# Kernel optimization log

Measured on AMD Instinct MI355X. Metric: run time of the kernel, lower is better.

## Reference

```python
import jax, jax.numpy as jnp
import numpy as np

N_NODES = 100000
N_EDGES = 1600000
N_GRAPHS = 512


def gcn_conv(x, W, b, src, dst, n_nodes):
    """GCNConv with self-loops: D^-1/2 (A+I) D^-1/2 X W + b."""
    h = x @ W  # [N, out]
    ones = jnp.ones((src.shape[0],), h.dtype)
    deg = jax.ops.segment_sum(ones, dst, num_segments=n_nodes) + 1.0  # +1 self-loop
    dinv = jax.lax.rsqrt(deg)
    norm = dinv[src] * dinv[dst]  # [E]
    agg = jax.ops.segment_sum(h[src] * norm[:, None], dst, num_segments=n_nodes)
    agg = agg + h * (1.0 / deg)[:, None]  # self-loop term: deg^-0.5 * deg^-0.5
    return agg + b


def setup_inputs() -> dict:
    key = jax.random.key(0)
    ks = jax.random.split(key, 12)
    x = jax.random.normal(ks[0], (N_NODES, 78), dtype=jnp.float32)
    edge_index = jax.random.randint(ks[1], (2, N_EDGES), 0, N_NODES, dtype=jnp.int64)
    batch = jnp.sort(jax.random.randint(ks[2], (N_NODES,), 0, N_GRAPHS, dtype=jnp.int64))
    def glorot(k, shape):
        lim = np.sqrt(6.0 / (shape[0] + shape[1])).astype(np.float32)
        return jax.random.uniform(k, shape, jnp.float32, -lim, lim)
    return {
        "x": x,
        "edge_index": edge_index,
        "batch": batch,
        "W1": glorot(ks[3], (78, 128)),
        "b1": jnp.zeros((128,), jnp.float32),
        "W2": glorot(ks[4], (128, 256)),
        "b2": jnp.zeros((256,), jnp.float32),
        "Wg1": glorot(ks[5], (256, 1024)),
        "bg1": jnp.zeros((1024,), jnp.float32),
        "Wg2": glorot(ks[6], (1024, 128)),
        "bg2": jnp.zeros((128,), jnp.float32),
    }


def reference(x, edge_index, batch, W1, b1, W2, b2, Wg1, bg1, Wg2, bg2):
    src, dst = edge_index[0], edge_index[1]
    n = x.shape[0]
    h = jax.nn.relu(gcn_conv(x, W1, b1, src, dst, n))   # [N,128]
    h = jax.nn.relu(gcn_conv(h, W2, b2, src, dst, n))   # [N,256]
    g = jax.ops.segment_max(h, batch, num_segments=N_GRAPHS)  # global max pool [G,256]
    g = jax.nn.relu(g @ Wg1 + bg1)   # [G,1024]; dropout is identity at eval
    g = g @ Wg2 + bg2                # [G,128]
    return g
```

## Files before the change

kernel.cpp:

```cpp
#include <hip/hip_runtime.h>
#include <hip/hip_fp16.h>


#define NN 100000
#define NE 1600000
#define NG 512
#define NBLK ((NN + 1023) / 1024)

typedef float v2f __attribute__((ext_vector_type(2)));


__global__ void k_hist(const int* __restrict__ dst, int* cnt, int e) {
    int i = blockIdx.x * blockDim.x + threadIdx.x;
    if (i < e) atomicAdd(&cnt[dst[i]], 1);
}

__global__ void k_prep(const int* __restrict__ cnt, float* __restrict__ dinv,
                       float* __restrict__ gmax) {
    int i = blockIdx.x * blockDim.x + threadIdx.x;
    if (i < NN) dinv[i] = rsqrtf((float)cnt[i] + 1.0f);
    if (i < NG * 256) gmax[i] = 0.0f;
}

__global__ void k_cvt_x(const float* __restrict__ x, __half* __restrict__ xh) {
    int i = blockIdx.x * blockDim.x + threadIdx.x;
    if (i < NN * 39) {
        float2 v = ((const float2*)x)[i];
        ((__half2*)xh)[i] = __floats2half2_rn(v.x, v.y);
    }
}

__global__ __launch_bounds__(256) void k_bsum(const int* __restrict__ cnt, int* __restrict__ bsum) {
    __shared__ int s[256];
    int b = blockIdx.x, t = threadIdx.x;
    int base = b * 1024 + t * 4;
    int v = 0;
#pragma unroll
    for (int j = 0; j < 4; j++) { int i = base + j; if (i < NN) v += cnt[i]; }
    s[t] = v; __syncthreads();
    for (int off = 128; off > 0; off >>= 1) {
        if (t < off) s[t] += s[t + off];
        __syncthreads();
    }
    if (t == 0) bsum[b] = s[0];
}

__global__ __launch_bounds__(128) void k_scan_bsum(int* bsum, int* row_ptr) {
    __shared__ int s[128];
    int t = threadIdx.x;
    int v = (t < NBLK) ? bsum[t] : 0;
    s[t] = v; __syncthreads();
    for (int off = 1; off < 128; off <<= 1) {
        int u = (t >= off) ? s[t - off] : 0;
        __syncthreads();
        s[t] += u;
        __syncthreads();
    }
    if (t < NBLK) bsum[t] = s[t] - v;
    if (t == 0) row_ptr[NN] = NE;
}

__global__ __launch_bounds__(256) void k_scan_blocks(const int* __restrict__ cnt,
    const int* __restrict__ bsum, int* __restrict__ row_ptr, int* __restrict__ cursor) {
    __shared__ int s[256];
    int b = blockIdx.x, t = threadIdx.x;
    int base = b * 1024 + t * 4;
    int v[4]; int sum = 0;
#pragma unroll
    for (int j = 0; j < 4; j++) { int i = base + j; v[j] = (i < NN) ? cnt[i] : 0; sum += v[j]; }
    s[t] = sum; __syncthreads();
    for (int off = 1; off < 256; off <<= 1) {
        int u = (t >= off) ? s[t - off] : 0;
        __syncthreads();
        s[t] += u;
        __syncthreads();
    }
    int excl = s[t] - sum + bsum[b];
#pragma unroll
    for (int j = 0; j < 4; j++) {
        int i = base + j;
        if (i < NN) { row_ptr[i] = excl; cursor[i] = excl; excl += v[j]; }
    }
}

__global__ void k_fillslots(const int* __restrict__ src, const int* __restrict__ dst,
    const float* __restrict__ dinv, int* cursor, int2* __restrict__ es, int e) {
    int i = blockIdx.x * blockDim.x + threadIdx.x;
    if (i >= e) return;
    int s = src[i], d = dst[i];
    int pos = atomicAdd(&cursor[d], 1);
    es[pos] = make_int2(s, __float_as_int(dinv[s] * dinv[d]));
}

__global__ __launch_bounds__(256) void k_fused1(const __half* __restrict__ x,
    const int* __restrict__ rp, const int2* __restrict__ es,
    const float* __restrict__ dinv, const float* __restrict__ W,
    const float* __restrict__ bias, __half* __restrict__ out) {
    __shared__ float As[4][8][80];
    int tid = threadIdx.x;
    int wv = tid >> 6, l = tid & 63;
    int task = __builtin_amdgcn_readfirstlane(blockIdx.x * 4 + wv);
    int n0 = task * 8;
    if (n0 >= NN) return;

    if (l < 39) {
        for (int pi = 0; pi < 4; pi++) {
            int nA = n0 + 2 * pi, nB = nA + 1;
            float diA = dinv[nA], swA = diA * diA;
            float diB = dinv[nB], swB = diB * diB;
            float2 aA = __half22float2(((const __half2*)(x + (size_t)nA * 78))[l]);
            float2 aB = __half22float2(((const __half2*)(x + (size_t)nB * 78))[l]);
            aA.x *= swA; aA.y *= swA;
            aB.x *= swB; aB.y *= swB;
            int eA = rp[nA], eA1 = rp[nA + 1];
            int eB = rp[nB], eB1 = rp[nB + 1];
            int cA = (eA1 - eA) >> 3, cB = (eB1 - eB) >> 3;
            while (cA > 0 || cB > 0) {
                bool dA = (cA > 0), dB = (cB > 0);
                int2 esA[8], esB[8];
                __half2 vA[8], vB[8];
                if (dA) {
#pragma unroll
                    for (int j = 0; j < 8; j++) esA[j] = es[eA + j];
                }
                if (dB) {
#pragma unroll
                    for (int j = 0; j < 8; j++) esB[j] = es[eB + j];
                }
                if (dA) {
#pragma unroll
                    for (int j = 0; j < 8; j++)
                        vA[j] = ((const __half2*)(x + (size_t)esA[j].x * 78))[l];
                }
                if (dB) {
#pragma unroll
                    for (int j = 0; j < 8; j++)
                        vB[j] = ((const __half2*)(x + (size_t)esB[j].x * 78))[l];
                }
                if (dA) {
#pragma unroll
                    for (int j = 0; j < 8; j++) {
                        float w = __int_as_float(esA[j].y);
                        float2 v = __half22float2(vA[j]);
                        aA.x += v.x * w; aA.y += v.y * w;
                    }
                    eA += 8; cA--;
                }
                if (dB) {
#pragma unroll
                    for (int j = 0; j < 8; j++) {
                        float w = __int_as_float(esB[j].y);
                        float2 v = __half22float2(vB[j]);
                        aB.x += v.x * w; aB.y += v.y * w;
                    }
                    eB += 8; cB--;
                }
            }
            while (eA < eA1 && eB < eB1) {
                int2 pA = es[eA], pB = es[eB];
                float2 vA2 = __half22float2(((const __half2*)(x + (size_t)pA.x * 78))[l]);
                float2 vB2 = __half22float2(((const __half2*)(x + (size_t)pB.x * 78))[l]);
                float wA = __int_as_float(pA.y), wB = __int_as_float(pB.y);
                aA.x += vA2.x * wA; aA.y += vA2.y * wA;
                aB.x += vB2.x * wB; aB.y += vB2.y * wB;
                eA++; eB++;
            }
            for (; eA < eA1; eA++) {
                int2 p = es[eA];
                float w = __int_as_float(p.y);
                float2 v = __half22float2(((const __half2*)(x + (size_t)p.x * 78))[l]);
                aA.x += v.x * w; aA.y += v.y * w;
            }
            for (; eB < eB1; eB++) {
                int2 p = es[eB];
                float w = __int_as_float(p.y);
                float2 v = __half22float2(((const __half2*)(x + (size_t)p.x * 78))[l]);
                aB.x += v.x * w; aB.y += v.y * w;
            }
            *(float2*)&As[wv][2 * pi][2 * l] = aA;
            *(float2*)&As[wv][2 * pi + 1][2 * l] = aB;
        }
    }

    int f0 = l * 2;
    float2 acc[8];
#pragma unroll
    for (int i = 0; i < 8; i++) acc[i] = make_float2(0.f, 0.f);

    for (int k = 0; k < 76; k += 4) {
        float2 w0 = *(const float2*)&W[(k + 0) * 128 + f0];
        float2 w1 = *(const float2*)&W[(k + 1) * 128 + f0];
        float2 w2 = *(const float2*)&W[(k + 2) * 128 + f0];
        float2 w3 = *(const float2*)&W[(k + 3) * 128 + f0];
#pragma unroll
        for (int i = 0; i < 8; i++) {
            float4 a = *(const float4*)&As[wv][i][k];
            acc[i].x += a.x * w0.x + a.y * w1.x + a.z * w2.x + a.w * w3.x;
            acc[i].y += a.x * w0.y + a.y * w1.y + a.z * w2.y + a.w * w3.y;
        }
    }
    {
        float2 w0 = *(const float2*)&W[76 * 128 + f0];
        float2 w1 = *(const float2*)&W[77 * 128 + f0];
#pragma unroll
        for (int i = 0; i < 8; i++) {
            float2 a = *(const float2*)&As[wv][i][76];
            acc[i].x += a.x * w0.x + a.y * w1.x;
            acc[i].y += a.x * w0.y + a.y * w1.y;
        }
    }
    float2 bv = *(const float2*)&bias[f0];
#pragma unroll
    for (int i = 0; i < 8; i++) {
        float ox = fmaxf(acc[i].x + bv.x, 0.f);
        float oy = fmaxf(acc[i].y + bv.y, 0.f);
        *(__half2*)&out[(size_t)(n0 + i) * 128 + f0] = __floats2half2_rn(ox, oy);
    }
}

__global__ __launch_bounds__(256) void k_fused2(const __half* __restrict__ h,
    const int* __restrict__ rp, const int2* __restrict__ es,
    const float* __restrict__ dinv, const float* __restrict__ W,
    const float* __restrict__ bias, const int* __restrict__ batch,
    unsigned* __restrict__ gmax) {
    __shared__ float As[4][8][128];
    int tid = threadIdx.x;
    int wv = tid >> 6, l = tid & 63;
    int task = __builtin_amdgcn_readfirstlane(blockIdx.x * 4 + wv);
    int n0 = task * 8;
    if (n0 >= NN) return;

    for (int pi = 0; pi < 4; pi++) {
        int nA = n0 + 2 * pi, nB = nA + 1;
        float diA = dinv[nA], swA = diA * diA;
        float diB = dinv[nB], swB = diB * diB;
        float2 aA = __half22float2(((const __half2*)(h + (size_t)nA * 128))[l]);
        float2 aB = __half22float2(((const __half2*)(h + (size_t)nB * 128))[l]);
        aA.x *= swA; aA.y *= swA;
        aB.x *= swB; aB.y *= swB;
        int eA = rp[nA], eA1 = rp[nA + 1];
        int eB = rp[nB], eB1 = rp[nB + 1];
        int cA = (eA1 - eA) >> 3, cB = (eB1 - eB) >> 3;
        while (cA > 0 || cB > 0) {
            bool dA = (cA > 0), dB = (cB > 0);
            int2 esA[8], esB[8];
            __half2 vA[8], vB[8];
            if (dA) {
#pragma unroll
                for (int j = 0; j < 8; j++) esA[j] = es[eA + j];
            }
            if (dB) {
#pragma unroll
                for (int j = 0; j < 8; j++) esB[j] = es[eB + j];
            }
            if (dA) {
#pragma unroll
                for (int j = 0; j < 8; j++)
                    vA[j] = ((const __half2*)(h + (size_t)esA[j].x * 128))[l];
            }
            if (dB) {
#pragma unroll
                for (int j = 0; j < 8; j++)
                    vB[j] = ((const __half2*)(h + (size_t)esB[j].x * 128))[l];
            }
            if (dA) {
#pragma unroll
                for (int j = 0; j < 8; j++) {
                    float w = __int_as_float(esA[j].y);
                    float2 v = __half22float2(vA[j]);
                    aA.x += v.x * w; aA.y += v.y * w;
                }
                eA += 8; cA--;
            }
            if (dB) {
#pragma unroll
                for (int j = 0; j < 8; j++) {
                    float w = __int_as_float(esB[j].y);
                    float2 v = __half22float2(vB[j]);
                    aB.x += v.x * w; aB.y += v.y * w;
                }
                eB += 8; cB--;
            }
        }
        while (eA < eA1 && eB < eB1) {
            int2 pA = es[eA], pB = es[eB];
            float2 vA2 = __half22float2(((const __half2*)(h + (size_t)pA.x * 128))[l]);
            float2 vB2 = __half22float2(((const __half2*)(h + (size_t)pB.x * 128))[l]);
            float wA = __int_as_float(pA.y), wB = __int_as_float(pB.y);
            aA.x += vA2.x * wA; aA.y += vA2.y * wA;
            aB.x += vB2.x * wB; aB.y += vB2.y * wB;
            eA++; eB++;
        }
        for (; eA < eA1; eA++) {
            int2 p = es[eA];
            float w = __int_as_float(p.y);
            float2 v = __half22float2(((const __half2*)(h + (size_t)p.x * 128))[l]);
            aA.x += v.x * w; aA.y += v.y * w;
        }
        for (; eB < eB1; eB++) {
            int2 p = es[eB];
            float w = __int_as_float(p.y);
            float2 v = __half22float2(((const __half2*)(h + (size_t)p.x * 128))[l]);
            aB.x += v.x * w; aB.y += v.y * w;
        }
        *(float2*)&As[wv][2 * pi][2 * l] = aA;
        *(float2*)&As[wv][2 * pi + 1][2 * l] = aB;
    }

    int f0 = l * 4;
    v2f acc[8][2];
#pragma unroll
    for (int i = 0; i < 8; i++) { acc[i][0] = (v2f)(0.f); acc[i][1] = (v2f)(0.f); }

    for (int k = 0; k < 128; k += 4) {
        float4 w0 = *(const float4*)&W[(size_t)(k + 0) * 256 + f0];
        float4 w1 = *(const float4*)&W[(size_t)(k + 1) * 256 + f0];
        float4 w2 = *(const float4*)&W[(size_t)(k + 2) * 256 + f0];
        float4 w3 = *(const float4*)&W[(size_t)(k + 3) * 256 + f0];
        v2f w0a = {w0.x, w0.y}, w0b = {w0.z, w0.w};
        v2f w1a = {w1.x, w1.y}, w1b = {w1.z, w1.w};
        v2f w2a = {w2.x, w2.y}, w2b = {w2.z, w2.w};
        v2f w3a = {w3.x, w3.y}, w3b = {w3.z, w3.w};
#pragma unroll
        for (int i = 0; i < 8; i++) {
            float4 a = *(const float4*)&As[wv][i][k];
            v2f sx = {a.x, a.x}, sy = {a.y, a.y}, sz = {a.z, a.z}, sw = {a.w, a.w};
            acc[i][0] = __builtin_elementwise_fma(sx, w0a, acc[i][0]);
            acc[i][1] = __builtin_elementwise_fma(sx, w0b, acc[i][1]);
            acc[i][0] = __builtin_elementwise_fma(sy, w1a, acc[i][0]);
            acc[i][1] = __builtin_elementwise_fma(sy, w1b, acc[i][1]);
            acc[i][0] = __builtin_elementwise_fma(sz, w2a, acc[i][0]);
            acc[i][1] = __builtin_elementwise_fma(sz, w2b, acc[i][1]);
            acc[i][0] = __builtin_elementwise_fma(sw, w3a, acc[i][0]);
            acc[i][1] = __builtin_elementwise_fma(sw, w3b, acc[i][1]);
        }
    }

    float4 bv = *(const float4*)&bias[f0];
    int curg = -1;
    float4 m = make_float4(0.f, 0.f, 0.f, 0.f);
#pragma unroll
    for (int i = 0; i < 8; i++) {
        int g = batch[n0 + i];
        float4 v;
        v.x = fmaxf(acc[i][0].x + bv.x, 0.f); v.y = fmaxf(acc[i][0].y + bv.y, 0.f);
        v.z = fmaxf(acc[i][1].x + bv.z, 0.f); v.w = fmaxf(acc[i][1].y + bv.w, 0.f);
        if (g != curg) {
            if (curg >= 0) {
                unsigned* gp = &gmax[(size_t)curg * 256 + f0];
                atomicMax(&gp[0], __float_as_uint(m.x));
                atomicMax(&gp[1], __float_as_uint(m.y));
                atomicMax(&gp[2], __float_as_uint(m.z));
                atomicMax(&gp[3], __float_as_uint(m.w));
            }
            curg = g; m = v;
        } else {
            m.x = fmaxf(m.x, v.x); m.y = fmaxf(m.y, v.y);
            m.z = fmaxf(m.z, v.z); m.w = fmaxf(m.w, v.w);
        }
    }
    if (curg >= 0) {
        unsigned* gp = &gmax[(size_t)curg * 256 + f0];
        atomicMax(&gp[0], __float_as_uint(m.x));
        atomicMax(&gp[1], __float_as_uint(m.y));
        atomicMax(&gp[2], __float_as_uint(m.z));
        atomicMax(&gp[3], __float_as_uint(m.w));
    }
}


__global__ __launch_bounds__(256) void k_gemm3(const float* __restrict__ A,
    const float* __restrict__ W, const float* __restrict__ bias,
    float* __restrict__ out) {
    __shared__ float rs[8][256];
    int b = blockIdx.x, tid = threadIdx.x;
#pragma unroll
    for (int g = 0; g < 8; g++) rs[g][tid] = A[(b * 8 + g) * 256 + tid];
    __syncthreads();
    float acc[8][4];
#pragma unroll
    for (int g = 0; g < 8; g++)
#pragma unroll
        for (int j = 0; j < 4; j++) acc[g][j] = 0.f;
    for (int k = 0; k < 256; k++) {
        float w0 = W[k * 1024 + tid];
        float w1 = W[k * 1024 + tid + 256];
        float w2 = W[k * 1024 + tid + 512];
        float w3 = W[k * 1024 + tid + 768];
#pragma unroll
        for (int g = 0; g < 8; g++) {
            float a = rs[g][k];
            acc[g][0] += a * w0; acc[g][1] += a * w1;
            acc[g][2] += a * w2; acc[g][3] += a * w3;
        }
    }
#pragma unroll
    for (int g = 0; g < 8; g++)
#pragma unroll
        for (int j = 0; j < 4; j++) {
            int f = tid + j * 256;
            out[(b * 8 + g) * 1024 + f] = fmaxf(acc[g][j] + bias[f], 0.0f);
        }
}

__global__ __launch_bounds__(128) void k_gemm4(const float* __restrict__ A,
    const float* __restrict__ W, const float* __restrict__ bias,
    float* __restrict__ out) {
    __shared__ float rs[4][1024];
    int b = blockIdx.x, tid = threadIdx.x;
    for (int i = tid; i < 4096; i += 128) rs[i >> 10][i & 1023] = A[b * 4096 + i];
    __syncthreads();
    float acc[4] = {0.f, 0.f, 0.f, 0.f};
    for (int k = 0; k < 1024; k++) {
        float wv = W[k * 128 + tid];
#pragma unroll
        for (int g = 0; g < 4; g++) acc[g] += rs[g][k] * wv;
    }
#pragma unroll
    for (int g = 0; g < 4; g++)
        out[(b * 4 + g) * 128 + tid] = acc[g] + bias[tid];
}

extern "C" void kernel_launch(void* const* d_in, const int* in_sizes, int n_in,
                              void* d_out, int out_size, void* d_ws, size_t ws_size,
                              hipStream_t stream) {
    const float* x    = (const float*)d_in[0];
    const int*   ei   = (const int*)d_in[1];
    const int*   batch= (const int*)d_in[2];
    const float* W1   = (const float*)d_in[3];
    const float* b1   = (const float*)d_in[4];
    const float* W2   = (const float*)d_in[5];
    const float* b2   = (const float*)d_in[6];
    const float* Wg1  = (const float*)d_in[7];
    const float* bg1  = (const float*)d_in[8];
    const float* Wg2  = (const float*)d_in[9];
    const float* bg2  = (const float*)d_in[10];
    const int* src = ei;
    const int* dst = ei + NE;

    char* w8 = (char*)d_ws;
    int*   cnt     = (int*)w8;                 w8 += (size_t)NN * 4;
    int*   row_ptr = (int*)w8;                 w8 += (size_t)(NN + 4) * 4;
    int*   cursor  = (int*)w8;                 w8 += (size_t)NN * 4;
    int*   bsum    = (int*)w8;                 w8 += 128 * 4;
    int2*  es      = (int2*)w8;                w8 += (size_t)NE * 8;
    float* dinv    = (float*)w8;               w8 += (size_t)NN * 4;
    __half* xh     = (__half*)w8;              w8 += (size_t)NN * 78 * 2;
    __half* h1     = (__half*)w8;              w8 += (size_t)NN * 128 * 2;
    unsigned* gmax = (unsigned*)w8;            w8 += (size_t)NG * 256 * 4;
    float* g1      = (float*)w8;               w8 += (size_t)NG * 1024 * 4;

    hipMemsetAsync(cnt, 0, (size_t)NN * 4, stream);
    k_hist<<<(NE + 255) / 256, 256, 0, stream>>>(dst, cnt, NE);
    k_cvt_x<<<(NN * 39 + 255) / 256, 256, 0, stream>>>(x, xh);
    k_prep<<<(NG * 256 + 255) / 256, 256, 0, stream>>>(cnt, dinv, (float*)gmax);
    k_bsum<<<NBLK, 256, 0, stream>>>(cnt, bsum);
    k_scan_bsum<<<1, 128, 0, stream>>>(bsum, row_ptr);
    k_scan_blocks<<<NBLK, 256, 0, stream>>>(cnt, bsum, row_ptr, cursor);
    k_fillslots<<<(NE + 255) / 256, 256, 0, stream>>>(src, dst, dinv, cursor, es, NE);

    k_fused1<<<NN / 32, 256, 0, stream>>>(xh, row_ptr, es, dinv, W1, b1, h1);

    k_fused2<<<NN / 32, 256, 0, stream>>>(h1, row_ptr, es, dinv, W2, b2, batch, gmax);

    k_gemm3<<<NG / 8, 256, 0, stream>>>((const float*)gmax, Wg1, bg1, g1);
    k_gemm4<<<NG / 4, 128, 0, stream>>>(g1, Wg2, bg2, (float*)d_out);
}
```

Measured before the change: 578.3 us.

## Use split-fp16 MFMA for the second GCN layer's dense transform

Replaces the FP32 FMA-based 128x256 dense transform in the second fused aggregation kernel with MFMA 16x16x32 f16 instructions. Both the aggregated activations and W2 are split into hi/lo half pairs, and three MFMAs per tile approximate FP32 accuracy. A new pre-pass packs W2 into the MFMA B-operand layout. Each wave now handles 16 nodes instead of 8, which halves the number of blocks, increases per-wave gather work and lowers parallelism for the latency-bound aggregation phase.

After: 618.2 us. 6.9% more time.

```diff
diff --git a/kernel.cpp b/kernel.cpp
--- a/kernel.cpp
+++ b/kernel.cpp
@@ -8,6 +8,8 @@
 #define NBLK ((NN + 1023) / 1024)
 
 typedef float v2f __attribute__((ext_vector_type(2)));
+typedef _Float16 half8 __attribute__((ext_vector_type(8)));
+typedef float f32x4 __attribute__((ext_vector_type(4)));
 
 
 __global__ void k_hist(const int* __restrict__ dst, int* cnt, int e) {
@@ -28,6 +30,19 @@
         float2 v = ((const float2*)x)[i];
         ((__half2*)xh)[i] = __floats2half2_rn(v.x, v.y);
     }
+}
+
+__global__ void k_pack_w2(const float* __restrict__ W, __half* __restrict__ Wh,
+                          __half* __restrict__ Wl) {
+    int i = blockIdx.x * blockDim.x + threadIdx.x;
+    if (i >= 32768) return;
+    int j = i & 7, lane = (i >> 3) & 63, ks = (i >> 9) & 3, nt = i >> 11;
+    int n = nt * 16 + (lane & 15);
+    int k = ks * 32 + ((lane >> 4) << 3) + j;
+    float v = W[k * 256 + n];
+    __half hi = __float2half_rn(v);
+    Wh[i] = hi;
+    Wl[i] = __float2half_rn(v - __half2float(hi));
 }
 
 __global__ __launch_bounds__(256) void k_bsum(const int* __restrict__ cnt, int* __restrict__ bsum) {
@@ -220,17 +235,18 @@
 
 __global__ __launch_bounds__(256) void k_fused2(const __half* __restrict__ h,
     const int* __restrict__ rp, const int2* __restrict__ es,
-    const float* __restrict__ dinv, const float* __restrict__ W,
-    const float* __restrict__ bias, const int* __restrict__ batch,
-    unsigned* __restrict__ gmax) {
-    __shared__ float As[4][8][128];
+    const float* __restrict__ dinv, const __half* __restrict__ W2h,
+    const __half* __restrict__ W2l, const float* __restrict__ bias,
+    const int* __restrict__ batch, unsigned* __restrict__ gmax) {
+    __shared__ __half Ah[4][16][128];
+    __shared__ __half Al[4][16][128];
     int tid = threadIdx.x;
     int wv = tid >> 6, l = tid & 63;
     int task = __builtin_amdgcn_readfirstlane(blockIdx.x * 4 + wv);
-    int n0 = task * 8;
-    if (n0 >= NN) return;
-
-    for (int pi = 0; pi < 4; pi++) {
+    if (task >= 6250) return;
+    int n0 = task * 16;
+
+    for (int pi = 0; pi < 8; pi++) {
         int nA = n0 + 2 * pi, nB = nA + 1;
         float diA = dinv[nA], swA = diA * diA;
         float diB = dinv[nB], swB = diB * diB;
@@ -303,68 +319,62 @@
             float2 v = __half22float2(((const __half2*)(h + (size_t)p.x * 128))[l]);
             aB.x += v.x * w; aB.y += v.y * w;
         }
-        *(float2*)&As[wv][2 * pi][2 * l] = aA;
-        *(float2*)&As[wv][2 * pi + 1][2 * l] = aB;
-    }
-
-    int f0 = l * 4;
-    v2f acc[8][2];
-#pragma unroll
-    for (int i = 0; i < 8; i++) { acc[i][0] = (v2f)(0.f); acc[i][1] = (v2f)(0.f); }
-
-    for (int k = 0; k < 128; k += 4) {
-        float4 w0 = *(const float4*)&W[(size_t)(k + 0) * 256 + f0];
-        float4 w1 = *(const float4*)&W[(size_t)(k + 1) * 256 + f0];
-        float4 w2 = *(const float4*)&W[(size_t)(k + 2) * 256 + f0];
-        float4 w3 = *(const float4*)&W[(size_t)(k + 3) * 256 + f0];
-        v2f w0a = {w0.x, w0.y}, w0b = {w0.z, w0.w};
-        v2f w1a = {w1.x, w1.y}, w1b = {w1.z, w1.w};
-        v2f w2a = {w2.x, w2.y}, w2b = {w2.z, w2.w};
-        v2f w3a = {w3.x, w3.y}, w3b = {w3.z, w3.w};
-#pragma unroll
-        for (int i = 0; i < 8; i++) {
-            float4 a = *(const float4*)&As[wv][i][k];
-            v2f sx = {a.x, a.x}, sy = {a.y, a.y}, sz = {a.z, a.z}, sw = {a.w, a.w};
-            acc[i][0] = __builtin_elementwise_fma(sx, w0a, acc[i][0]);
-            acc[i][1] = __builtin_elementwise_fma(sx, w0b, acc[i][1]);
-            acc[i][0] = __builtin_elementwise_fma(sy, w1a, acc[i][0]);
-            acc[i][1] = __builtin_elementwise_fma(sy, w1b, acc[i][1]);
-            acc[i][0] = __builtin_elementwise_fma(sz, w2a, acc[i][0]);
-            acc[i][1] = __builtin_elementwise_fma(sz, w2b, acc[i][1]);
-            acc[i][0] = __builtin_elementwise_fma(sw, w3a, acc[i][0]);
-            acc[i][1] = __builtin_elementwise_fma(sw, w3b, acc[i][1]);
-        }
-    }
-
-    float4 bv = *(const float4*)&bias[f0];
-    int curg = -1;
-    float4 m = make_float4(0.f, 0.f, 0.f, 0.f);
-#pragma unroll
-    for (int i = 0; i < 8; i++) {
-        int g = batch[n0 + i];
-        float4 v;
-        v.x = fmaxf(acc[i][0].x + bv.x, 0.f); v.y = fmaxf(acc[i][0].y + bv.y, 0.f);
-        v.z = fmaxf(acc[i][1].x + bv.z, 0.f); v.w = fmaxf(acc[i][1].y + bv.w, 0.f);
-        if (g != curg) {
-            if (curg >= 0) {
-                unsigned* gp = &gmax[(size_t)curg * 256 + f0];
-                atomicMax(&gp[0], __float_as_uint(m.x));
-                atomicMax(&gp[1], __float_as_uint(m.y));
-                atomicMax(&gp[2], __float_as_uint(m.z));
-                atomicMax(&gp[3], __float_as_uint(m.w));
-            }
-            curg = g; m = v;
-        } else {
-            m.x = fmaxf(m.x, v.x); m.y = fmaxf(m.y, v.y);
-            m.z = fmaxf(m.z, v.z); m.w = fmaxf(m.w, v.w);
-        }
-    }
-    if (curg >= 0) {
-        unsigned* gp = &gmax[(size_t)curg * 256 + f0];
-        atomicMax(&gp[0], __float_as_uint(m.x));
-        atomicMax(&gp[1], __float_as_uint(m.y));
-        atomicMax(&gp[2], __float_as_uint(m.z));
-        atomicMax(&gp[3], __float_as_uint(m.w));
+        __half2 hiA = __floats2half2_rn(aA.x, aA.y);
+        float2 bkA = __half22float2(hiA);
+        __half2 loA = __floats2half2_rn(aA.x - bkA.x, aA.y - bkA.y);
+        __half2 hiB = __floats2half2_rn(aB.x, aB.y);
+        float2 bkB = __half22float2(hiB);
+        __half2 loB = __floats2half2_rn(aB.x - bkB.x, aB.y - bkB.y);
+        *(__half2*)&Ah[wv][2 * pi][2 * l] = hiA;
+        *(__half2*)&Al[wv][2 * pi][2 * l] = loA;
+        *(__half2*)&Ah[wv][2 * pi + 1][2 * l] = hiB;
+        *(__half2*)&Al[wv][2 * pi + 1][2 * l] = loB;
+    }
+
+    int row4 = (l >> 4) << 2;
+    int gg[4];
+#pragma unroll
+    for (int r = 0; r < 4; r++) gg[r] = batch[n0 + row4 + r];
+    int am = l & 15;
+    int akb = ((l >> 4) << 3);
+
+    for (int hh = 0; hh < 2; hh++) {
+        f32x4 acc[8];
+#pragma unroll
+        for (int i = 0; i < 8; i++) acc[i] = (f32x4)(0.f);
+#pragma unroll
+        for (int ks = 0; ks < 4; ks++) {
+            half8 ah = *(const half8*)&Ah[wv][am][ks * 32 + akb];
+            half8 al = *(const half8*)&Al[wv][am][ks * 32 + akb];
+#pragma unroll
+            for (int nt = 0; nt < 8; nt++) {
+                int fi = ((((hh * 8 + nt) * 4 + ks) * 64) + l) * 8;
+                half8 bh = *(const half8*)&W2h[fi];
+                half8 bl = *(const half8*)&W2l[fi];
+                acc[nt] = __builtin_amdgcn_mfma_f32_16x16x32_f16(ah, bh, acc[nt], 0, 0, 0);
+                acc[nt] = __builtin_amdgcn_mfma_f32_16x16x32_f16(ah, bl, acc[nt], 0, 0, 0);
+                acc[nt] = __builtin_amdgcn_mfma_f32_16x16x32_f16(al, bh, acc[nt], 0, 0, 0);
+            }
+        }
+#pragma unroll
+        for (int nt = 0; nt < 8; nt++) {
+            int n = (hh * 8 + nt) * 16 + am;
+            float bv = bias[n];
+            int curg = -1;
+            float m = 0.f;
+#pragma unroll
+            for (int r = 0; r < 4; r++) {
+                int g = gg[r];
+                float v = fmaxf(acc[nt][r] + bv, 0.f);
+                if (g != curg) {
+                    if (curg >= 0) atomicMax(&gmax[(size_t)curg * 256 + n], __float_as_uint(m));
+                    curg = g; m = v;
+                } else {
+                    m = fmaxf(m, v);
+                }
+            }
+            if (curg >= 0) atomicMax(&gmax[(size_t)curg * 256 + n], __float_as_uint(m));
+        }
     }
 }
 
@@ -447,12 +457,15 @@
     float* dinv    = (float*)w8;               w8 += (size_t)NN * 4;
     __half* xh     = (__half*)w8;              w8 += (size_t)NN * 78 * 2;
     __half* h1     = (__half*)w8;              w8 += (size_t)NN * 128 * 2;
+    __half* w2h    = (__half*)w8;              w8 += 32768 * 2;
+    __half* w2l    = (__half*)w8;              w8 += 32768 * 2;
     unsigned* gmax = (unsigned*)w8;            w8 += (size_t)NG * 256 * 4;
     float* g1      = (float*)w8;               w8 += (size_t)NG * 1024 * 4;
 
     hipMemsetAsync(cnt, 0, (size_t)NN * 4, stream);
     k_hist<<<(NE + 255) / 256, 256, 0, stream>>>(dst, cnt, NE);
     k_cvt_x<<<(NN * 39 + 255) / 256, 256, 0, stream>>>(x, xh);
+    k_pack_w2<<<128, 256, 0, stream>>>(W2, w2h, w2l);
     k_prep<<<(NG * 256 + 255) / 256, 256, 0, stream>>>(cnt, dinv, (float*)gmax);
     k_bsum<<<NBLK, 256, 0, stream>>>(cnt, bsum);
     k_scan_bsum<<<1, 128, 0, stream>>>(bsum, row_ptr);
@@ -461,7 +474,7 @@
 
     k_fused1<<<NN / 32, 256, 0, stream>>>(xh, row_ptr, es, dinv, W1, b1, h1);
 
-    k_fused2<<<NN / 32, 256, 0, stream>>>(h1, row_ptr, es, dinv, W2, b2, batch, gmax);
+    k_fused2<<<(6250 + 3) / 4, 256, 0, stream>>>(h1, row_ptr, es, dinv, w2h, w2l, b2, batch, gmax);
 
     k_gemm3<<<NG / 8, 256, 0, stream>>>((const float*)gmax, Wg1, bg1, g1);
     k_gemm4<<<NG / 4, 128, 0, stream>>>(g1, Wg2, bg2, (float*)d_out);
```
